# Kernel tuning notes

Measured on AMD Instinct MI355X. Metric: run time of the kernel, lower is better.

Reference implementation:

```python
import jax, jax.numpy as jnp
import numpy as np

B, S, NX, NH = 4, 1024, 1024, 16
HD = NX // NH  # head_features = 64


def setup_inputs() -> dict:
    key = jax.random.key(0)
    k1, k2, k3 = jax.random.split(key, 3)
    x = jax.random.normal(k1, (B, S, NX), dtype=jnp.float32)
    w_attn = 0.02 * jax.random.normal(k2, (NX, 3 * NX), dtype=jnp.float32)
    b_attn = jnp.zeros((3 * NX,), dtype=jnp.float32)
    w_proj = 0.02 * jax.random.normal(k3, (NX, NX), dtype=jnp.float32)
    b_proj = jnp.zeros((NX,), dtype=jnp.float32)
    causal_bias = jnp.tril(jnp.ones((S, S), dtype=jnp.float32))  # tril buffer
    return {"x": x, "w_attn": w_attn, "b_attn": b_attn,
            "w_proj": w_proj, "b_proj": b_proj, "causal_bias": causal_bias}


def reference(x, w_attn, b_attn, w_proj, b_proj, causal_bias):
    # c_attn: fused qkv projection (Conv1D == addmm)
    qkv = x @ w_attn + b_attn                     # [B, S, 3*NX]
    q, k, v = jnp.split(qkv, 3, axis=-1)          # each [B, S, NX]
    # split heads -> [B, H, S, D]
    q = q.reshape(B, S, NH, HD).transpose(0, 2, 1, 3)
    k = k.reshape(B, S, NH, HD).transpose(0, 2, 1, 3)
    v = v.reshape(B, S, NH, HD).transpose(0, 2, 1, 3)
    # present: stack of (key in [B,H,S,D] layout, value)
    present = jnp.stack((k, v))                   # [2, B, H, S, D]
    # scores with scale=True
    w = jnp.einsum('bhqd,bhkd->bhqk', q, k) / jnp.sqrt(jnp.float32(HD))
    b = causal_bias[None, None, :, :]             # [1,1,S,S] (nd==ns==S)
    w = w * b - 1e10 * (1.0 - b)                  # multiplicative mask trick
    p = jax.nn.softmax(w, axis=-1)
    a = jnp.einsum('bhqk,bhkd->bhqd', p, v)       # [B, H, S, D]
    a = a.transpose(0, 2, 1, 3).reshape(B, S, NX)  # merge heads
    out = a @ w_proj + b_proj                     # c_proj
    return out, present
```

## Files before the change

kernel.cpp:

```cpp
#include <hip/hip_runtime.h>
#include <hip/hip_bf16.h>

typedef __attribute__((ext_vector_type(8))) short short8;
typedef __attribute__((ext_vector_type(4))) float floatx4;

constexpr int Bsz = 4, Ssz = 1024, NXc = 1024, NHc = 16, HDc = 64;
constexpr int OUT_ELEMS  = Bsz * Ssz * NXc;
constexpr int HEAD_ELEMS = Bsz * NHc * Ssz * HDc;

union BF8 { __hip_bfloat16 h[8]; uint4 v; short8 s; };

__device__ __forceinline__ uint4 cvt8(const float* __restrict__ p) {
    float4 a = *reinterpret_cast<const float4*>(p);
    float4 b = *reinterpret_cast<const float4*>(p + 4);
    BF8 u;
    u.h[0] = __float2bfloat16(a.x); u.h[1] = __float2bfloat16(a.y);
    u.h[2] = __float2bfloat16(a.z); u.h[3] = __float2bfloat16(a.w);
    u.h[4] = __float2bfloat16(b.x); u.h[5] = __float2bfloat16(b.y);
    u.h[6] = __float2bfloat16(b.z); u.h[7] = __float2bfloat16(b.w);
    return u.v;
}

__device__ __forceinline__ void load_lds_16B(const void* g, void* l) {
    __builtin_amdgcn_global_load_lds(
        (const __attribute__((address_space(1))) unsigned int*)g,
        (__attribute__((address_space(3))) unsigned int*)l, 16, 0, 0);
}


__global__ __launch_bounds__(256) void cvt_kernel(
    const float* __restrict__ in, __hip_bfloat16* __restrict__ out, int n)
{
    int i = (blockIdx.x * 256 + threadIdx.x) * 8;
    if (i < n)
        *reinterpret_cast<uint4*>(out + i) = cvt8(in + i);
}

__global__ __launch_bounds__(256) void transpose_cvt(
    const float* __restrict__ in, __hip_bfloat16* __restrict__ out,
    int K, int N)
{
    __shared__ float t[64][65];
    const int tid = threadIdx.x;
    const int k0 = blockIdx.y * 64, n0 = blockIdx.x * 64;
#pragma unroll
    for (int j = 0; j < 16; ++j) {
        const int idx = tid + j * 256;
        const int row = idx >> 6, col = idx & 63;
        t[row][col] = in[(size_t)(k0 + row) * N + n0 + col];
    }
    __syncthreads();
#pragma unroll
    for (int j = 0; j < 16; ++j) {
        const int idx = tid + j * 256;
        const int orow = idx >> 6, ocol = idx & 63;
        out[(size_t)(n0 + orow) * K + k0 + ocol] = __float2bfloat16(t[ocol][orow]);
    }
}

template <int EPI>
__global__ __launch_bounds__(256) void gemm128(
    const __hip_bfloat16* __restrict__ A,
    const __hip_bfloat16* __restrict__ Bt,
    const float* __restrict__ bias,
    float* __restrict__ outf,
    __hip_bfloat16* __restrict__ qws,
    float* __restrict__ present,
    int M, int N, int K)
{
    __shared__ __align__(16) __hip_bfloat16 As[128 * 32];
    __shared__ __align__(16) __hip_bfloat16 Bs[128 * 32];

    const int tid  = threadIdx.x;
    const int w    = tid >> 6, lane = tid & 63;
    const int quad = lane >> 4, l16 = lane & 15;
    const int m0 = blockIdx.y * 128, n0 = blockIdx.x * 128;
    const int mb = (w >> 1) * 64, nbw = (w & 1) * 64;

    const int srow = lane >> 2;
    const int skseg = (lane & 3) * 8;

    floatx4 acc[4][4];
#pragma unroll
    for (int i = 0; i < 4; ++i)
#pragma unroll
        for (int j = 0; j < 4; ++j)
#pragma unroll
            for (int r = 0; r < 4; ++r) acc[i][j][r] = 0.f;

    for (int k0 = 0; k0 < K; k0 += 32) {
#pragma unroll
        for (int c = 0; c < 2; ++c) {
            const int chunk = w * 2 + c;
            const int row = chunk * 16 + srow;
            load_lds_16B(A + (size_t)(m0 + row) * K + k0 + skseg,
                         &As[chunk * 512]);
            load_lds_16B(Bt + (size_t)(n0 + row) * K + k0 + skseg,
                         &Bs[chunk * 512]);
        }
        __syncthreads();

        short8 af[4], bfr[4];
#pragma unroll
        for (int mi = 0; mi < 4; ++mi)
            af[mi] = *reinterpret_cast<const short8*>(
                &As[(mb + mi * 16 + l16) * 32 + quad * 8]);
#pragma unroll
        for (int ni = 0; ni < 4; ++ni)
            bfr[ni] = *reinterpret_cast<const short8*>(
                &Bs[(nbw + ni * 16 + l16) * 32 + quad * 8]);
#pragma unroll
        for (int mi = 0; mi < 4; ++mi)
#pragma unroll
            for (int ni = 0; ni < 4; ++ni)
                acc[mi][ni] = __builtin_amdgcn_mfma_f32_16x16x32_bf16(
                    af[mi], bfr[ni], acc[mi][ni], 0, 0, 0);

        __syncthreads();
    }

#pragma unroll
    for (int mi = 0; mi < 4; ++mi) {
#pragma unroll
        for (int ni = 0; ni < 4; ++ni) {
            const int col = n0 + nbw + ni * 16 + l16;
            const float bsv = bias[col];
#pragma unroll
            for (int r = 0; r < 4; ++r) {
                const int row = m0 + mb + mi * 16 + quad * 4 + r;
                const float v = acc[mi][ni][r] + bsv;
                if (EPI == 0) {
                    const int seg = col >> 10;
                    const int c = col & 1023;
                    if (seg == 0) {
                        qws[(size_t)row * 1024 + c] = __float2bfloat16(v);
                    } else {
                        const int b = row >> 10, s = row & 1023;
                        const int h = c >> 6, d = c & 63;
                        const size_t idx =
                            ((size_t)((b * 16 + h) * 1024 + s)) * 64 + d;
                        if (seg == 1) present[idx] = v;
                        else          present[HEAD_ELEMS + idx] = v;
                    }
                } else {
                    outf[(size_t)row * N + col] = v;
                }
            }
        }
    }
}

__global__ __launch_bounds__(256) void repack_kv(
    const float* __restrict__ present,
    __hip_bfloat16* __restrict__ k_ws,
    __hip_bfloat16* __restrict__ vt_ws)
{
    const int kt = blockIdx.x;
    const int bh = blockIdx.y;
    const int tid = threadIdx.x;
    const size_t toff = ((size_t)bh * 1024 + kt * 64) * 64;
    const float* Kp = present + toff;
    const float* Vp = present + HEAD_ELEMS + toff;
    __hip_bfloat16* ko = k_ws  + ((size_t)bh * 16 + kt) * 4096;
    __hip_bfloat16* vo = vt_ws + ((size_t)bh * 16 + kt) * 4096;

    __shared__ float Vt[64][65];

    const int row = tid >> 3, seg = tid & 7;
#pragma unroll
    for (int it = 0; it < 2; ++it) {
        const int r = row + it * 32;
        *reinterpret_cast<uint4*>(&ko[r * 64 + ((seg ^ (r & 7)) << 3)]) =
            cvt8(Kp + (size_t)r * 64 + seg * 8);
        const float* vp = Vp + (size_t)r * 64 + seg * 8;
        float4 v0 = *reinterpret_cast<const float4*>(vp);
        float4 v1 = *reinterpret_cast<const float4*>(vp + 4);
        Vt[seg * 8 + 0][r] = v0.x; Vt[seg * 8 + 1][r] = v0.y;
        Vt[seg * 8 + 2][r] = v0.z; Vt[seg * 8 + 3][r] = v0.w;
        Vt[seg * 8 + 4][r] = v1.x; Vt[seg * 8 + 5][r] = v1.y;
        Vt[seg * 8 + 6][r] = v1.z; Vt[seg * 8 + 7][r] = v1.w;
    }
    __syncthreads();
#pragma unroll
    for (int it = 0; it < 2; ++it) {
        const int d = row + it * 32;
        BF8 u;
#pragma unroll
        for (int i = 0; i < 8; ++i)
            u.h[i] = __float2bfloat16(Vt[d][seg * 8 + i]);
        *reinterpret_cast<uint4*>(&vo[d * 64 + ((seg ^ (d & 7)) << 3)]) = u.v;
    }
}

__global__ __launch_bounds__(256) void attn_v4(
    const __hip_bfloat16* __restrict__ q_ws,
    const __hip_bfloat16* __restrict__ k_ws,
    const __hip_bfloat16* __restrict__ vt_ws,
    __hip_bfloat16* __restrict__ a_ws)
{
    const int bx = blockIdx.x, h = blockIdx.y, b = blockIdx.z;
    const int tid  = threadIdx.x;
    const int wave = tid >> 6, lane = tid & 63;
    const int quad = lane >> 4, l16 = lane & 15;
    const int stripe = wave * 16;

    const int bh = b * 16 + h;
    const __hip_bfloat16* Kbase = k_ws  + (size_t)bh * 65536;
    const __hip_bfloat16* Vbase = vt_ws + (size_t)bh * 65536;

    __shared__ __align__(16) __hip_bfloat16 Ksf[3][4096];
    __shared__ __align__(16) __hip_bfloat16 Vsf[3][4096];
    __shared__ __align__(16) __hip_bfloat16 Ps[64][72];

#pragma unroll
    for (int pass = 0; pass < 2; ++pass) {
        const int qt = (pass == 0) ? (8 + bx) : (7 - bx);

        const __hip_bfloat16* Qb =
            q_ws + ((size_t)(b * Ssz + qt * 64 + stripe + l16)) * NXc + h * 64;
        const short8 qf0 = *reinterpret_cast<const short8*>(Qb + quad * 8);
        const short8 qf1 = *reinterpret_cast<const short8*>(Qb + 32 + quad * 8);

        float m_i[4], l_i[4];
#pragma unroll
        for (int r = 0; r < 4; ++r) { m_i[r] = -1e9f; l_i[r] = 0.f; }
        floatx4 oacc[4];
#pragma unroll
        for (int ni = 0; ni < 4; ++ni)
#pragma unroll
            for (int r = 0; r < 4; ++r) oacc[ni][r] = 0.f;

#pragma unroll
        for (int c2 = 0; c2 < 2; ++c2) {
            const int c = wave + c2 * 4;
            load_lds_16B(Kbase + c * 512 + (lane << 3), &Ksf[0][c * 512]);
            load_lds_16B(Vbase + c * 512 + (lane << 3), &Vsf[0][c * 512]);
        }

        int cw = 0;
        for (int kt = 0; kt <= qt; ++kt) {
            if (kt < qt) {
                const int nb_ = (cw == 2) ? 0 : cw + 1;
                const __hip_bfloat16* Kt = Kbase + (size_t)(kt + 1) * 4096;
                const __hip_bfloat16* Vt = Vbase + (size_t)(kt + 1) * 4096;
#pragma unroll
                for (int c2 = 0; c2 < 2; ++c2) {
                    const int c = wave + c2 * 4;
                    load_lds_16B(Kt + c * 512 + (lane << 3), &Ksf[nb_][c * 512]);
                    load_lds_16B(Vt + c * 512 + (lane << 3), &Vsf[nb_][c * 512]);
                }
                asm volatile("s_waitcnt vmcnt(4)" ::: "memory");
            } else {
                asm volatile("s_waitcnt vmcnt(0)" ::: "memory");
            }
            __builtin_amdgcn_s_barrier();
            __builtin_amdgcn_sched_barrier(0);

            floatx4 sacc[4];
#pragma unroll
            for (int ni = 0; ni < 4; ++ni)
#pragma unroll
                for (int r = 0; r < 4; ++r) sacc[ni][r] = 0.f;
            __builtin_amdgcn_s_setprio(1);
#pragma unroll
            for (int ni = 0; ni < 4; ++ni) {
                const int key = ni * 16 + l16;
                const int sw = key & 7;
                const short8 kf0 = *reinterpret_cast<const short8*>(
                    &Ksf[cw][key * 64 + ((quad ^ sw) << 3)]);
                const short8 kf1 = *reinterpret_cast<const short8*>(
                    &Ksf[cw][key * 64 + (((4 + quad) ^ sw) << 3)]);
                sacc[ni] = __builtin_amdgcn_mfma_f32_16x16x32_bf16(
                    qf0, kf0, sacc[ni], 0, 0, 0);
                sacc[ni] = __builtin_amdgcn_mfma_f32_16x16x32_bf16(
                    qf1, kf1, sacc[ni], 0, 0, 0);
            }
            __builtin_amdgcn_s_setprio(0);

            const bool diag = (kt == qt);
            float alpha_[4];
#pragma unroll
            for (int r = 0; r < 4; ++r) {
                const int lrow = stripe + quad * 4 + r;
                float sv[4];
                float mx = -1e30f;
#pragma unroll
                for (int ni = 0; ni < 4; ++ni) {
                    float v = sacc[ni][r] * 0.125f;
                    if (diag && (ni * 16 + l16) > lrow) v = -1e9f;
                    sv[ni] = v;
                    mx = fmaxf(mx, v);
                }
                mx = fmaxf(mx, __shfl_xor(mx, 1));
                mx = fmaxf(mx, __shfl_xor(mx, 2));
                mx = fmaxf(mx, __shfl_xor(mx, 4));
                mx = fmaxf(mx, __shfl_xor(mx, 8));
                const float mnew = fmaxf(m_i[r], mx);
                const float al = __expf(m_i[r] - mnew);
                m_i[r] = mnew;
                float s = 0.f;
#pragma unroll
                for (int nn = 0; nn < 4; ++nn) {
                    const int ni = (nn + quad) & 3;
                    const float p = __expf(sv[ni] - mnew);
                    s += p;
                    Ps[lrow][ni * 16 + l16] = __float2bfloat16(p);
                }
                s += __shfl_xor(s, 1);
                s += __shfl_xor(s, 2);
                s += __shfl_xor(s, 4);
                s += __shfl_xor(s, 8);
                l_i[r] = l_i[r] * al + s;
                alpha_[r] = al;
            }

#pragma unroll
            for (int ni = 0; ni < 4; ++ni)
#pragma unroll
                for (int r = 0; r < 4; ++r) oacc[ni][r] *= alpha_[r];

            __builtin_amdgcn_s_setprio(1);
#pragma unroll
            for (int kk = 0; kk < 64; kk += 32) {
                const short8 pf = *reinterpret_cast<const short8*>(
                    &Ps[stripe + l16][kk + quad * 8]);
#pragma unroll
                for (int ni = 0; ni < 4; ++ni) {
                    const int d = ni * 16 + l16;
                    const int chunk = (kk >> 3) + quad;
                    const short8 vf = *reinterpret_cast<const short8*>(
                        &Vsf[cw][d * 64 + ((chunk ^ (d & 7)) << 3)]);
                    oacc[ni] = __builtin_amdgcn_mfma_f32_16x16x32_bf16(
                        pf, vf, oacc[ni], 0, 0, 0);
                }
            }
            __builtin_amdgcn_s_setprio(0);

            cw = (cw == 2) ? 0 : cw + 1;
        }

        __builtin_amdgcn_s_barrier();

#pragma unroll
        for (int ni = 0; ni < 4; ++ni) {
#pragma unroll
            for (int r = 0; r < 4; ++r) {
                const int row = qt * 64 + stripe + quad * 4 + r;
                const int col = h * 64 + ni * 16 + l16;
                const float inv = 1.0f / fmaxf(l_i[r], 1e-20f);
                a_ws[((size_t)(b * Ssz + row)) * NXc + col] =
                    __float2bfloat16(oacc[ni][r] * inv);
            }
        }
    }
}

template <int EPI>
__global__ __launch_bounds__(256) void gemm64(
    const void* __restrict__ Av, const float* __restrict__ Bw,
    const float* __restrict__ bias, float* __restrict__ out0,
    float* __restrict__ present, int M, int N, int K)
{
    __shared__ __align__(16) __hip_bfloat16 As[64][40];
    __shared__ __align__(16) __hip_bfloat16 Bs[64][40];
    const int tid = threadIdx.x;
    const int wave = tid >> 6, lane = tid & 63;
    const int quad = lane >> 4, l16 = lane & 15;
    const int m0 = blockIdx.y * 64, n0 = blockIdx.x * 64;
    const int mb = (wave >> 1) * 32, nb = (wave & 1) * 32;
    const int arow = tid >> 2, aseg = tid & 3;
    const int brow = tid >> 3, bseg = tid & 7;
    floatx4 acc[2][2];
#pragma unroll
    for (int i = 0; i < 2; ++i)
#pragma unroll
        for (int j = 0; j < 2; ++j)
#pragma unroll
            for (int r = 0; r < 4; ++r) acc[i][j][r] = 0.f;
    for (int k0 = 0; k0 < K; k0 += 32) {
        if (EPI == 0) {
            const float* A = (const float*)Av;
            *reinterpret_cast<uint4*>(&As[arow][aseg * 8]) =
                cvt8(A + (size_t)(m0 + arow) * K + k0 + aseg * 8);
        } else {
            const __hip_bfloat16* A = (const __hip_bfloat16*)Av;
            *reinterpret_cast<uint4*>(&As[arow][aseg * 8]) =
                *reinterpret_cast<const uint4*>(
                    A + (size_t)(m0 + arow) * K + k0 + aseg * 8);
        }
        const float* bp = Bw + (size_t)(k0 + brow) * N + n0 + bseg * 8;
        float4 b0 = *reinterpret_cast<const float4*>(bp);
        float4 b1 = *reinterpret_cast<const float4*>(bp + 4);
        Bs[bseg * 8 + 0][brow] = __float2bfloat16(b0.x);
        Bs[bseg * 8 + 1][brow] = __float2bfloat16(b0.y);
        Bs[bseg * 8 + 2][brow] = __float2bfloat16(b0.z);
        Bs[bseg * 8 + 3][brow] = __float2bfloat16(b0.w);
        Bs[bseg * 8 + 4][brow] = __float2bfloat16(b1.x);
        Bs[bseg * 8 + 5][brow] = __float2bfloat16(b1.y);
        Bs[bseg * 8 + 6][brow] = __float2bfloat16(b1.z);
        Bs[bseg * 8 + 7][brow] = __float2bfloat16(b1.w);
        __syncthreads();
        short8 af[2], bf[2];
#pragma unroll
        for (int mm = 0; mm < 2; ++mm)
            af[mm] = *reinterpret_cast<const short8*>(&As[mb + mm * 16 + l16][quad * 8]);
#pragma unroll
        for (int nn = 0; nn < 2; ++nn)
            bf[nn] = *reinterpret_cast<const short8*>(&Bs[nb + nn * 16 + l16][quad * 8]);
#pragma unroll
        for (int mm = 0; mm < 2; ++mm)
#pragma unroll
            for (int nn = 0; nn < 2; ++nn)
                acc[mm][nn] = __builtin_amdgcn_mfma_f32_16x16x32_bf16(
                    af[mm], bf[nn], acc[mm][nn], 0, 0, 0);
        __syncthreads();
    }
#pragma unroll
    for (int mm = 0; mm < 2; ++mm)
#pragma unroll
        for (int nn = 0; nn < 2; ++nn) {
            const int col = n0 + nb + nn * 16 + l16;
            const float bsv = bias[col];
#pragma unroll
            for (int r = 0; r < 4; ++r) {
                const int row = m0 + mb + mm * 16 + quad * 4 + r;
                const float v = acc[mm][nn][r] + bsv;
                if (EPI == 0) {
                    const int seg = col >> 10;
                    const int c = col & 1023;
                    if (seg == 0) out0[(size_t)row * 1024 + c] = v;
                    else {
                        const int b = row >> 10, s = row & 1023;
                        const int h = c >> 6, d = c & 63;
                        const size_t idx = ((size_t)((b * 16 + h) * 1024 + s)) * 64 + d;
                        if (seg == 1) present[idx] = v;
                        else          present[HEAD_ELEMS + idx] = v;
                    }
                } else out0[(size_t)row * N + col] = v;
            }
        }
}

__global__ __launch_bounds__(256) void attn64(
    const float* __restrict__ qbuf, const float* __restrict__ present,
    __hip_bfloat16* __restrict__ a_ws)
{
    const int qt = blockIdx.x, h = blockIdx.y, b = blockIdx.z;
    const int tid = threadIdx.x;
    const int wave = tid >> 6, lane = tid & 63;
    const int quad = lane >> 4, l16 = lane & 15;
    const int mb = (wave >> 1) * 32, nb = (wave & 1) * 32;
    const size_t headoff = ((size_t)(b * 16 + h)) * Ssz * HDc;
    const float* Qb = qbuf + ((size_t)(b * Ssz + qt * 64)) * NXc + h * 64;
    const float* Kp = present + headoff;
    const float* Vp = present + HEAD_ELEMS + headoff;
    __shared__ __align__(16) __hip_bfloat16 Qs[64][72];
    __shared__ __align__(16) __hip_bfloat16 Ks[64][72];
    __shared__ __align__(16) __hip_bfloat16 Vts[64][72];
    __shared__ __align__(16) __hip_bfloat16 Ps[64][72];
    __shared__ float Sc[64][65];
    __shared__ float mrow[64], lrow[64], arw[64];
#pragma unroll
    for (int it = 0; it < 2; ++it) {
        const int c = tid + it * 256;
        const int row = c >> 3, seg = c & 7;
        *reinterpret_cast<uint4*>(&Qs[row][seg * 8]) =
            cvt8(Qb + (size_t)row * NXc + seg * 8);
    }
    if (tid < 64) { mrow[tid] = -1e9f; lrow[tid] = 0.f; }
    floatx4 oacc[2][2];
#pragma unroll
    for (int i = 0; i < 2; ++i)
#pragma unroll
        for (int j = 0; j < 2; ++j)
#pragma unroll
            for (int r = 0; r < 4; ++r) oacc[i][j][r] = 0.f;
    __syncthreads();
    for (int kt = 0; kt <= qt; ++kt) {
#pragma unroll
        for (int it = 0; it < 2; ++it) {
            const int c = tid + it * 256;
            const int row = c >> 3, seg = c & 7;
            *reinterpret_cast<uint4*>(&Ks[row][seg * 8]) =
                cvt8(Kp + (size_t)(kt * 64 + row) * 64 + seg * 8);
            const float* vp = Vp + (size_t)(kt * 64 + row) * 64 + seg * 8;
            float4 v0 = *reinterpret_cast<const float4*>(vp);
            float4 v1 = *reinterpret_cast<const float4*>(vp + 4);
            Vts[seg * 8 + 0][row] = __float2bfloat16(v0.x);
            Vts[seg * 8 + 1][row] = __float2bfloat16(v0.y);
            Vts[seg * 8 + 2][row] = __float2bfloat16(v0.z);
            Vts[seg * 8 + 3][row] = __float2bfloat16(v0.w);
            Vts[seg * 8 + 4][row] = __float2bfloat16(v1.x);
            Vts[seg * 8 + 5][row] = __float2bfloat16(v1.y);
            Vts[seg * 8 + 6][row] = __float2bfloat16(v1.z);
            Vts[seg * 8 + 7][row] = __float2bfloat16(v1.w);
        }
        __syncthreads();
        floatx4 sacc[2][2];
#pragma unroll
        for (int i = 0; i < 2; ++i)
#pragma unroll
            for (int j = 0; j < 2; ++j)
#pragma unroll
                for (int r = 0; r < 4; ++r) sacc[i][j][r] = 0.f;
#pragma unroll
        for (int kd = 0; kd < 64; kd += 32) {
            short8 af[2], bf[2];
#pragma unroll
            for (int mm = 0; mm < 2; ++mm)
                af[mm] = *reinterpret_cast<const short8*>(&Qs[mb + mm * 16 + l16][kd + quad * 8]);
#pragma unroll
            for (int nn = 0; nn < 2; ++nn)
                bf[nn] = *reinterpret_cast<const short8*>(&Ks[nb + nn * 16 + l16][kd + quad * 8]);
#pragma unroll
            for (int mm = 0; mm < 2; ++mm)
#pragma unroll
                for (int nn = 0; nn < 2; ++nn)
                    sacc[mm][nn] = __builtin_amdgcn_mfma_f32_16x16x32_bf16(
                        af[mm], bf[nn], sacc[mm][nn], 0, 0, 0);
        }
        const bool diag = (kt == qt);
#pragma unroll
        for (int mm = 0; mm < 2; ++mm)
#pragma unroll
            for (int nn = 0; nn < 2; ++nn)
#pragma unroll
                for (int r = 0; r < 4; ++r) {
                    const int row = mb + mm * 16 + quad * 4 + r;
                    const int col = nb + nn * 16 + l16;
                    float v = fminf(fmaxf(sacc[mm][nn][r] * 0.125f, -1e8f), 1e8f);
                    if (diag && col > row) v = -1e9f;
                    Sc[row][col] = v;
                }
        __syncthreads();
        if (tid < 64) {
            const int r = tid;
            const float mo = mrow[r];
            float mx = mo;
            for (int c = 0; c < 64; ++c) mx = fmaxf(mx, Sc[r][c]);
            const float al = (mo <= -5e8f) ? 0.f : __expf(mo - mx);
            float sum = 0.f;
            for (int c = 0; c < 64; ++c) {
                const float sv = Sc[r][c];
                const float p = (sv <= -5e8f) ? 0.f : __expf(sv - mx);
                sum += p;
                Ps[r][c] = __float2bfloat16(p);
            }
            mrow[r] = mx;
            lrow[r] = lrow[r] * al + sum;
            arw[r]  = al;
        }
        __syncthreads();
#pragma unroll
        for (int mm = 0; mm < 2; ++mm) {
            const int rbase = mb + mm * 16 + quad * 4;
#pragma unroll
            for (int r = 0; r < 4; ++r) {
                const float al = arw[rbase + r];
                oacc[mm][0][r] *= al;
                oacc[mm][1][r] *= al;
            }
        }
#pragma unroll
        for (int kk = 0; kk < 64; kk += 32) {
            short8 pf[2], vf[2];
#pragma unroll
            for (int mm = 0; mm < 2; ++mm)
                pf[mm] = *reinterpret_cast<const short8*>(&Ps[mb + mm * 16 + l16][kk + quad * 8]);
#pragma unroll
            for (int nn = 0; nn < 2; ++nn)
                vf[nn] = *reinterpret_cast<const short8*>(&Vts[nb + nn * 16 + l16][kk + quad * 8]);
#pragma unroll
            for (int mm = 0; mm < 2; ++mm)
#pragma unroll
                for (int nn = 0; nn < 2; ++nn)
                    oacc[mm][nn] = __builtin_amdgcn_mfma_f32_16x16x32_bf16(
                        pf[mm], vf[nn], oacc[mm][nn], 0, 0, 0);
        }
        __syncthreads();
    }
#pragma unroll
    for (int mm = 0; mm < 2; ++mm)
#pragma unroll
        for (int nn = 0; nn < 2; ++nn)
#pragma unroll
            for (int r = 0; r < 4; ++r) {
                const int row = mb + mm * 16 + quad * 4 + r;
                const int col = nb + nn * 16 + l16;
                const float inv = 1.0f / fmaxf(lrow[row], 1e-20f);
                a_ws[((size_t)(b * Ssz + qt * 64 + row)) * NXc + h * 64 + col] =
                    __float2bfloat16(oacc[mm][nn][r] * inv);
            }
}

extern "C" void kernel_launch(void* const* d_in, const int* in_sizes, int n_in,
                              void* d_out, int out_size, void* d_ws, size_t ws_size,
                              hipStream_t stream) {
    const float* x      = (const float*)d_in[0];
    const float* w_attn = (const float*)d_in[1];
    const float* b_attn = (const float*)d_in[2];
    const float* w_proj = (const float*)d_in[3];
    const float* b_proj = (const float*)d_in[4];

    float* out     = (float*)d_out;
    float* present = out + OUT_ELEMS;

    const size_t NEED = 32u * 1024u * 1024u;
    if (ws_size >= NEED) {
        __hip_bfloat16* reg1 = (__hip_bfloat16*)d_ws;
        __hip_bfloat16* reg2 = reg1 + 4194304;
        __hip_bfloat16* reg3 = reg2 + 4194304;
        __hip_bfloat16* wTa  = reg3 + 4194304;
        __hip_bfloat16* wTp  = wTa + 3145728;

        cvt_kernel<<<2048, 256, 0, stream>>>(x, reg1, OUT_ELEMS);
        transpose_cvt<<<dim3(48, 16), 256, 0, stream>>>(w_attn, wTa, 1024, 3072);
        transpose_cvt<<<dim3(16, 16), 256, 0, stream>>>(w_proj, wTp, 1024, 1024);

        gemm128<0><<<dim3(24, 32), 256, 0, stream>>>(
            reg1, wTa, b_attn, nullptr, reg2, present, 4096, 3072, 1024);

        repack_kv<<<dim3(16, 64), 256, 0, stream>>>(present, reg3, reg1);

        attn_v4<<<dim3(8, 16, 4), 256, 0, stream>>>(reg2, reg3, reg1, reg2);

        gemm128<1><<<dim3(8, 32), 256, 0, stream>>>(
            reg2, wTp, b_proj, out, nullptr, nullptr, 4096, 1024, 1024);
    } else {
        __hip_bfloat16* a_ws = (__hip_bfloat16*)d_ws;
        hipMemsetAsync(d_ws, 0, (size_t)OUT_ELEMS * sizeof(__hip_bfloat16), stream);
        gemm64<0><<<dim3(48, 64), 256, 0, stream>>>(x, w_attn, b_attn, out, present,
                                                    4096, 3072, 1024);
        attn64<<<dim3(16, 16, 4), 256, 0, stream>>>(out, present, a_ws);
        gemm64<1><<<dim3(16, 64), 256, 0, stream>>>(a_ws, w_proj, b_proj, out, nullptr,
                                                    4096, 1024, 1024);
    }
}
```

Measured before the change: 213.9 us.

## Fuse K/V repack into QKV GEMM epilogue, triple-buffer GEMM, merge prep kernels

Merges the x conversion and both weight transpose-conversions into one prep launch. Adds a three-stage LDS ring to the bf16 GEMM with asynchronous global-to-LDS loads, waitcnt-based sync and raised priority around the MFMAs, replacing the two full barriers per k-step. The QKV GEMM epilogue now writes swizzled bf16 K and transposed V tiles directly, into the output buffer as scratch, which removes the separate repack kernel and its re-read of present. The trade-off is scattered 2-byte epilogue stores and more LDS per block.

```diff
diff --git a/kernel.cpp b/kernel.cpp
--- a/kernel.cpp
+++ b/kernel.cpp
@@ -28,21 +28,22 @@
 }
 
 
-__global__ __launch_bounds__(256) void cvt_kernel(
-    const float* __restrict__ in, __hip_bfloat16* __restrict__ out, int n)
+__global__ __launch_bounds__(256) void prep_kernel(
+    const float* __restrict__ x, __hip_bfloat16* __restrict__ x_bf,
+    const float* __restrict__ w_attn, __hip_bfloat16* __restrict__ wTa,
+    const float* __restrict__ w_proj, __hip_bfloat16* __restrict__ wTp)
 {
-    int i = (blockIdx.x * 256 + threadIdx.x) * 8;
-    if (i < n)
-        *reinterpret_cast<uint4*>(out + i) = cvt8(in + i);
-}
-
-__global__ __launch_bounds__(256) void transpose_cvt(
-    const float* __restrict__ in, __hip_bfloat16* __restrict__ out,
-    int K, int N)
-{
+    const int bid = blockIdx.x, tid = threadIdx.x;
     __shared__ float t[64][65];
-    const int tid = threadIdx.x;
-    const int k0 = blockIdx.y * 64, n0 = blockIdx.x * 64;
+    if (bid < 2048) {
+        const int i = (bid * 256 + tid) * 8;
+        *reinterpret_cast<uint4*>(x_bf + i) = cvt8(x + i);
+        return;
+    }
+    const float* in; __hip_bfloat16* outp; int N, bx, by;
+    if (bid < 2816) { const int q = bid - 2048; in = w_attn; outp = wTa; N = 3072; bx = q % 48; by = q / 48; }
+    else            { const int q = bid - 2816; in = w_proj; outp = wTp; N = 1024; bx = q % 16; by = q / 16; }
+    const int k0 = by * 64, n0 = bx * 64;
 #pragma unroll
     for (int j = 0; j < 16; ++j) {
         const int idx = tid + j * 256;
@@ -54,22 +55,24 @@
     for (int j = 0; j < 16; ++j) {
         const int idx = tid + j * 256;
         const int orow = idx >> 6, ocol = idx & 63;
-        out[(size_t)(n0 + orow) * K + k0 + ocol] = __float2bfloat16(t[ocol][orow]);
+        outp[(size_t)(n0 + orow) * 1024 + k0 + ocol] = __float2bfloat16(t[ocol][orow]);
     }
 }
 
 template <int EPI>
-__global__ __launch_bounds__(256) void gemm128(
+__global__ __launch_bounds__(256) void gemm128p(
     const __hip_bfloat16* __restrict__ A,
     const __hip_bfloat16* __restrict__ Bt,
     const float* __restrict__ bias,
     float* __restrict__ outf,
     __hip_bfloat16* __restrict__ qws,
     float* __restrict__ present,
+    __hip_bfloat16* __restrict__ kws,
+    __hip_bfloat16* __restrict__ vtws,
     int M, int N, int K)
 {
-    __shared__ __align__(16) __hip_bfloat16 As[128 * 32];
-    __shared__ __align__(16) __hip_bfloat16 Bs[128 * 32];
+    __shared__ __align__(16) __hip_bfloat16 As[3][4096];
+    __shared__ __align__(16) __hip_bfloat16 Bs[3][4096];
 
     const int tid  = threadIdx.x;
     const int w    = tid >> 6, lane = tid & 63;
@@ -88,35 +91,50 @@
 #pragma unroll
             for (int r = 0; r < 4; ++r) acc[i][j][r] = 0.f;
 
-    for (int k0 = 0; k0 < K; k0 += 32) {
+    auto stage = [&](int buf, int k0) {
 #pragma unroll
         for (int c = 0; c < 2; ++c) {
             const int chunk = w * 2 + c;
             const int row = chunk * 16 + srow;
             load_lds_16B(A + (size_t)(m0 + row) * K + k0 + skseg,
-                         &As[chunk * 512]);
+                         &As[buf][chunk * 512]);
             load_lds_16B(Bt + (size_t)(n0 + row) * K + k0 + skseg,
-                         &Bs[chunk * 512]);
-        }
-        __syncthreads();
+                         &Bs[buf][chunk * 512]);
+        }
+    };
+
+    stage(0, 0);
+    int cb = 0;
+    for (int k0 = 0; k0 < K; k0 += 32) {
+        if (k0 + 32 < K) {
+            const int nb_ = (cb == 2) ? 0 : cb + 1;
+            stage(nb_, k0 + 32);
+            asm volatile("s_waitcnt vmcnt(4)" ::: "memory");
+        } else {
+            asm volatile("s_waitcnt vmcnt(0)" ::: "memory");
+        }
+        __builtin_amdgcn_s_barrier();
+        __builtin_amdgcn_sched_barrier(0);
 
         short8 af[4], bfr[4];
 #pragma unroll
         for (int mi = 0; mi < 4; ++mi)
             af[mi] = *reinterpret_cast<const short8*>(
-                &As[(mb + mi * 16 + l16) * 32 + quad * 8]);
+                &As[cb][(mb + mi * 16 + l16) * 32 + quad * 8]);
 #pragma unroll
         for (int ni = 0; ni < 4; ++ni)
             bfr[ni] = *reinterpret_cast<const short8*>(
-                &Bs[(nbw + ni * 16 + l16) * 32 + quad * 8]);
+                &Bs[cb][(nbw + ni * 16 + l16) * 32 + quad * 8]);
+        __builtin_amdgcn_s_setprio(1);
 #pragma unroll
         for (int mi = 0; mi < 4; ++mi)
 #pragma unroll
             for (int ni = 0; ni < 4; ++ni)
                 acc[mi][ni] = __builtin_amdgcn_mfma_f32_16x16x32_bf16(
                     af[mi], bfr[ni], acc[mi][ni], 0, 0, 0);
-
-        __syncthreads();
+        __builtin_amdgcn_s_setprio(0);
+
+        cb = (cb == 2) ? 0 : cb + 1;
     }
 
 #pragma unroll
@@ -135,60 +153,30 @@
                     if (seg == 0) {
                         qws[(size_t)row * 1024 + c] = __float2bfloat16(v);
                     } else {
-                        const int b = row >> 10, s = row & 1023;
-                        const int h = c >> 6, d = c & 63;
+                        const int bq = row >> 10, s = row & 1023;
+                        const int hh = c >> 6, d = c & 63;
                         const size_t idx =
-                            ((size_t)((b * 16 + h) * 1024 + s)) * 64 + d;
-                        if (seg == 1) present[idx] = v;
-                        else          present[HEAD_ELEMS + idx] = v;
+                            ((size_t)((bq * 16 + hh) * 1024 + s)) * 64 + d;
+                        const int kt = s >> 6, key = s & 63;
+                        const size_t tbase =
+                            ((size_t)((bq * 16 + hh) * 16 + kt)) * 4096;
+                        if (seg == 1) {
+                            present[idx] = v;
+                            kws[tbase + key * 64 +
+                                ((((d >> 3) ^ (key & 7)) << 3) | (d & 7))] =
+                                __float2bfloat16(v);
+                        } else {
+                            present[HEAD_ELEMS + idx] = v;
+                            vtws[tbase + d * 64 +
+                                ((((key >> 3) ^ (d & 7)) << 3) | (key & 7))] =
+                                __float2bfloat16(v);
+                        }
                     }
                 } else {
                     outf[(size_t)row * N + col] = v;
                 }
             }
         }
-    }
-}
-
-__global__ __launch_bounds__(256) void repack_kv(
-    const float* __restrict__ present,
-    __hip_bfloat16* __restrict__ k_ws,
-    __hip_bfloat16* __restrict__ vt_ws)
-{
-    const int kt = blockIdx.x;
-    const int bh = blockIdx.y;
-    const int tid = threadIdx.x;
-    const size_t toff = ((size_t)bh * 1024 + kt * 64) * 64;
-    const float* Kp = present + toff;
-    const float* Vp = present + HEAD_ELEMS + toff;
-    __hip_bfloat16* ko = k_ws  + ((size_t)bh * 16 + kt) * 4096;
-    __hip_bfloat16* vo = vt_ws + ((size_t)bh * 16 + kt) * 4096;
-
-    __shared__ float Vt[64][65];
-
-    const int row = tid >> 3, seg = tid & 7;
-#pragma unroll
-    for (int it = 0; it < 2; ++it) {
-        const int r = row + it * 32;
-        *reinterpret_cast<uint4*>(&ko[r * 64 + ((seg ^ (r & 7)) << 3)]) =
-            cvt8(Kp + (size_t)r * 64 + seg * 8);
-        const float* vp = Vp + (size_t)r * 64 + seg * 8;
-        float4 v0 = *reinterpret_cast<const float4*>(vp);
-        float4 v1 = *reinterpret_cast<const float4*>(vp + 4);
-        Vt[seg * 8 + 0][r] = v0.x; Vt[seg * 8 + 1][r] = v0.y;
-        Vt[seg * 8 + 2][r] = v0.z; Vt[seg * 8 + 3][r] = v0.w;
-        Vt[seg * 8 + 4][r] = v1.x; Vt[seg * 8 + 5][r] = v1.y;
-        Vt[seg * 8 + 6][r] = v1.z; Vt[seg * 8 + 7][r] = v1.w;
-    }
-    __syncthreads();
-#pragma unroll
-    for (int it = 0; it < 2; ++it) {
-        const int d = row + it * 32;
-        BF8 u;
-#pragma unroll
-        for (int i = 0; i < 8; ++i)
-            u.h[i] = __float2bfloat16(Vt[d][seg * 8 + i]);
-        *reinterpret_cast<uint4*>(&vo[d * 64 + ((seg ^ (d & 7)) << 3)]) = u.v;
     }
 }
 
@@ -612,20 +600,20 @@
         __hip_bfloat16* reg3 = reg2 + 4194304;
         __hip_bfloat16* wTa  = reg3 + 4194304;
         __hip_bfloat16* wTp  = wTa + 3145728;
-
-        cvt_kernel<<<2048, 256, 0, stream>>>(x, reg1, OUT_ELEMS);
-        transpose_cvt<<<dim3(48, 16), 256, 0, stream>>>(w_attn, wTa, 1024, 3072);
-        transpose_cvt<<<dim3(16, 16), 256, 0, stream>>>(w_proj, wTp, 1024, 1024);
-
-        gemm128<0><<<dim3(24, 32), 256, 0, stream>>>(
-            reg1, wTa, b_attn, nullptr, reg2, present, 4096, 3072, 1024);
-
-        repack_kv<<<dim3(16, 64), 256, 0, stream>>>(present, reg3, reg1);
-
-        attn_v4<<<dim3(8, 16, 4), 256, 0, stream>>>(reg2, reg3, reg1, reg2);
-
-        gemm128<1><<<dim3(8, 32), 256, 0, stream>>>(
-            reg2, wTp, b_proj, out, nullptr, nullptr, 4096, 1024, 1024);
+        __hip_bfloat16* kws  = (__hip_bfloat16*)out;
+        __hip_bfloat16* vtws = kws + 4194304;
+
+        prep_kernel<<<3072, 256, 0, stream>>>(x, reg1, w_attn, wTa, w_proj, wTp);
+
+        gemm128p<0><<<dim3(24, 32), 256, 0, stream>>>(
+            reg1, wTa, b_attn, nullptr, reg2, present, kws, vtws,
+            4096, 3072, 1024);
+
+        attn_v4<<<dim3(8, 16, 4), 256, 0, stream>>>(reg2, kws, vtws, reg2);
+
+        gemm128p<1><<<dim3(8, 32), 256, 0, stream>>>(
+            reg2, wTp, b_proj, out, nullptr, nullptr, nullptr, nullptr,
+            4096, 1024, 1024);
     } else {
         __hip_bfloat16* a_ws = (__hip_bfloat16*)d_ws;
         hipMemsetAsync(d_ws, 0, (size_t)OUT_ELEMS * sizeof(__hip_bfloat16), stream);
```

Measured after the change: 194.9 us. -8.9%, faster.
